# Kernel tuning notes

Hardware: AMD Instinct MI355X
Metric: run time of the kernel (lower is better)

Reference implementation:

```python
import jax, jax.numpy as jnp
import numpy as np

NUM_HEADS = 16


def setup_inputs() -> dict:
    key = jax.random.key(0)
    ks = jax.random.split(key, 7)
    B, L, H = 4, 1370, 1024
    s = 0.02
    return {
        "hidden_states": jax.random.normal(ks[0], (B, L, H), jnp.float32),
        "Wq": jax.random.normal(ks[1], (H, H), jnp.float32) * s,
        "bq": jax.random.normal(ks[2], (H,), jnp.float32) * s,
        "Wk": jax.random.normal(ks[3], (H, H), jnp.float32) * s,
        "bk": jax.random.normal(ks[4], (H,), jnp.float32) * s,
        "Wv": jax.random.normal(ks[5], (H, H), jnp.float32) * s,
        "bv": jax.random.normal(ks[6], (H,), jnp.float32) * s,
    }


def reference(hidden_states, Wq, bq, Wk, bk, Wv, bv):
    B, L, hidden = hidden_states.shape
    n_heads = NUM_HEADS
    d = hidden // n_heads  # head_dim = 64

    def split_heads(x):  # [B,L,hidden] -> [B,H,L,d]
        return x.reshape(B, L, n_heads, d).transpose(0, 2, 1, 3)

    # torch Linear: y = x @ W^T + b
    q = split_heads(hidden_states @ Wq.T + bq)
    k = split_heads(hidden_states @ Wk.T + bk)
    v = split_heads(hidden_states @ Wv.T + bv)

    scale = 1.0 / jnp.sqrt(jnp.asarray(d, hidden_states.dtype))
    # attn_bias is all-zeros (no causal mask, no head_mask) -> omitted
    scores = jnp.einsum("bhld,bhsd->bhls", q, k) * scale  # [B,H,L,S]
    attn = jax.nn.softmax(scores, axis=-1)
    # dropout_p = 0.0 (eval mode), callback is None
    ctx = jnp.einsum("bhls,bhsd->bhld", attn, v)  # [B,H,L,d]
    ctx = ctx.transpose(0, 2, 1, 3).reshape(B, L, hidden)
    return ctx
```

## Files before the change

### kernel.cpp

```cpp
#include <hip/hip_runtime.h>

#define B_    4
#define L_    1370
#define NH_   16
#define D_    64
#define HID_  1024
#define M_    (B_ * L_)
#define LPAD  1408

#define XB_OFF  0u
#define WB_OFF  5611520u
#define QW_OFF  8757248u
#define KW_OFF  14524416u
#define VT_OFF  20291584u

typedef __attribute__((ext_vector_type(8))) short bf16x8;
typedef __attribute__((ext_vector_type(4))) short bf16x4;
typedef __attribute__((ext_vector_type(4))) float f32x4;
typedef __attribute__((ext_vector_type(2))) unsigned int u32x2;

#define LOG2E   1.44269504089f
#define QSCALE  0.18033688011f
#define SOFT_M2 14.4269504089f

__device__ __forceinline__ unsigned short f2bf(float f) {
  unsigned int u = __builtin_bit_cast(unsigned int, f);
  u += 0x7FFFu + ((u >> 16) & 1u);
  return (unsigned short)(u >> 16);
}

__device__ __forceinline__ float fexp2(float x) {
#if __has_builtin(__builtin_amdgcn_exp2f)
  return __builtin_amdgcn_exp2f(x);
#else
  return exp2f(x);
#endif
}

__device__ __forceinline__ unsigned int pkbf(float a, float b) {
#if __has_builtin(__builtin_amdgcn_cvt_pk_bf16_f32)
  auto r = __builtin_amdgcn_cvt_pk_bf16_f32(a, b);
  return __builtin_bit_cast(unsigned int, r);
#else
  return (unsigned int)f2bf(a) | ((unsigned int)f2bf(b) << 16);
#endif
}

#define GLOAD16(gp, lp)                                                    \
  __builtin_amdgcn_global_load_lds(                                        \
      (const __attribute__((address_space(1))) unsigned int*)(gp),         \
      (__attribute__((address_space(3))) unsigned int*)(lp), 16, 0, 0)

#define XN4 ((M_ * HID_) / 4)
#define WN4 ((HID_ * HID_) / 4)
#define TOT4 (XN4 + 3 * WN4)

__global__ void cvt_all(const float* __restrict__ hs,
                        const float* __restrict__ Wq,
                        const float* __restrict__ Wk,
                        const float* __restrict__ Wv,
                        unsigned short* __restrict__ ws) {
  int i4 = blockIdx.x * 256 + threadIdx.x;
  if (i4 >= TOT4) return;
  const float* src;
  unsigned short* dst;
  if (i4 < XN4) {
    src = hs + (size_t)i4 * 4;
    dst = ws + XB_OFF + (size_t)i4 * 4;
  } else {
    int j = i4 - XN4;
    int w = j >> 18;
    int jj = j & (WN4 - 1);
    src = (w == 0 ? Wq : w == 1 ? Wk : Wv) + (size_t)jj * 4;
    dst = ws + WB_OFF + (size_t)w * (HID_ * HID_) + (size_t)jj * 4;
  }
  float4 v = *(const float4*)src;
  bf16x4 o;
  o[0] = (short)f2bf(v.x); o[1] = (short)f2bf(v.y);
  o[2] = (short)f2bf(v.z); o[3] = (short)f2bf(v.w);
  *(bf16x4*)dst = o;
}

__global__ __launch_bounds__(256)
void qkv_gemm(const unsigned short* __restrict__ XB,
              const unsigned short* __restrict__ WB,
              const float* __restrict__ bq,
              const float* __restrict__ bk,
              const float* __restrict__ bv,
              unsigned short* __restrict__ ws) {
  __shared__ unsigned short smem[32768];

  const int x = blockIdx.x;
  const int b = (x >= 33) ? 3 : (x >= 22) ? 2 : (x >= 11) ? 1 : 0;
  const int j = x - 11 * b;
  const int z = blockIdx.z;
  const int n0 = blockIdx.y * 128;

  const unsigned short* W = WB + (size_t)z * (HID_ * HID_);
  const float* bias = (z == 0) ? bq : (z == 1) ? bk : bv;
  const float scale = (z == 0) ? QSCALE : 1.0f;

  const int tid = threadIdx.x;
  const int lane = tid & 63;
  const int wv = tid >> 6;
  const int l15 = lane & 15, quad = lane >> 4;
  const int wr = wv >> 1, wc = wv & 1;

  const int srow = (lane >> 3);
  const int gsw = (lane & 7) ^ srow;
  int offA[4], offB[4];
#pragma unroll
  for (int i = 0; i < 4; ++i) {
    int row = wv * 32 + 8 * i + srow;
    int m = b * L_ + min(j * 128 + row, L_ - 1);
    offA[i] = m * HID_ + gsw * 8;
    offB[i] = (n0 + row) * HID_ + gsw * 8;
  }

  f32x4 acc[4][4];
#pragma unroll
  for (int i = 0; i < 4; i++)
#pragma unroll
    for (int jj = 0; jj < 4; jj++) acc[i][jj] = (f32x4){0.f, 0.f, 0.f, 0.f};

#pragma unroll
  for (int i = 0; i < 4; ++i) {
    GLOAD16(XB + offA[i], &smem[(wv * 32 + 8 * i) * 64]);
    GLOAD16(W + offB[i], &smem[8192 + (wv * 32 + 8 * i) * 64]);
  }

  for (int kt = 0; kt < HID_ / 64; ++kt) {
    __syncthreads();
    unsigned short* cur = smem + (kt & 1) * 16384;
    if (kt + 1 < HID_ / 64) {
      unsigned short* nxt = smem + ((kt + 1) & 1) * 16384;
      const int ko = (kt + 1) * 64;
#pragma unroll
      for (int i = 0; i < 4; ++i) {
        GLOAD16(XB + offA[i] + ko, &nxt[(wv * 32 + 8 * i) * 64]);
        GLOAD16(W + offB[i] + ko, &nxt[8192 + (wv * 32 + 8 * i) * 64]);
      }
    }
    const unsigned short* lA = cur;
    const unsigned short* lB = cur + 8192;
#pragma unroll
    for (int kk = 0; kk < 2; ++kk) {
      bf16x8 af[4], bfr[4];
#pragma unroll
      for (int mi = 0; mi < 4; mi++) {
        int row = wr * 64 + mi * 16 + l15;
        af[mi] = *(const bf16x8*)&lA[row * 64 + (((kk * 4 + quad) ^ (l15 & 7)) * 8)];
      }
#pragma unroll
      for (int ni = 0; ni < 4; ni++) {
        int row = wc * 64 + ni * 16 + l15;
        bfr[ni] = *(const bf16x8*)&lB[row * 64 + (((kk * 4 + quad) ^ (l15 & 7)) * 8)];
      }
#pragma unroll
      for (int mi = 0; mi < 4; mi++)
#pragma unroll
        for (int ni = 0; ni < 4; ni++)
          acc[mi][ni] = __builtin_amdgcn_mfma_f32_16x16x32_bf16(af[mi], bfr[ni], acc[mi][ni], 0, 0, 0);
    }
  }

  __syncthreads();
  unsigned short* lC = smem + wv * 4096;
  const int h = blockIdx.y * 2 + wc;
  const int bh = b * 16 + h;
  const int lbase = j * 128 + wr * 64;

  if (z < 2) {
#pragma unroll
    for (int ni = 0; ni < 4; ni++) {
      int nl = ni * 16 + l15;
      float bn = bias[n0 + wc * 64 + nl];
      int gsn = nl >> 3, en = nl & 7;
#pragma unroll
      for (int mi = 0; mi < 4; mi++)
#pragma unroll
        for (int r = 0; r < 4; r++) {
          int ml = mi * 16 + quad * 4 + r;
          lC[ml * 64 + ((gsn ^ (ml & 7)) * 8) + en] = f2bf((acc[mi][ni][r] + bn) * scale);
        }
    }
    unsigned short* dst = ws + (z == 0 ? QW_OFF : KW_OFF) + (size_t)bh * (LPAD * 64);
#pragma unroll
    for (int i = 0; i < 8; ++i) {
      int ml = i * 8 + (lane >> 3);
      int g = lane & 7;
      bf16x8 v = *(const bf16x8*)&lC[ml * 64 + ((g ^ (ml & 7)) * 8)];
      int l = lbase + ml;
      *(bf16x8*)(dst + (size_t)l * 64 + g * 8) = v;
    }
  } else {
#pragma unroll
    for (int ni = 0; ni < 4; ni++) {
      int nl = ni * 16 + l15;
      float bn = bias[n0 + wc * 64 + nl];
#pragma unroll
      for (int mi = 0; mi < 4; mi++) {
        bf16x4 pk;
#pragma unroll
        for (int r = 0; r < 4; r++) pk[r] = (short)f2bf(acc[mi][ni][r] + bn);
        int gm = mi * 2 + (quad >> 1), h2 = quad & 1;
        *(bf16x4*)&lC[nl * 64 + ((gm ^ (nl & 7)) * 8) + h2 * 4] = pk;
      }
    }
    unsigned short* vt = ws + VT_OFF + (size_t)bh * (64 * LPAD);
#pragma unroll
    for (int i = 0; i < 8; ++i) {
      int nl = i * 8 + (lane >> 3);
      int g = lane & 7;
      bf16x8 v = *(const bf16x8*)&lC[nl * 64 + ((g ^ (nl & 7)) * 8)];
      int l = lbase + g * 8;
      *(bf16x8*)(vt + (size_t)nl * LPAD + l) = v;
    }
  }
}

__global__ __launch_bounds__(256)
void attn(const unsigned short* __restrict__ ws, float* __restrict__ out) {
  __shared__ unsigned short lKV[2 * 8192];
  __shared__ unsigned short lP[4 * 32 * 64];

  const int tid = threadIdx.x;
  const int qt = blockIdx.x >> 3;
  const int bh = blockIdx.y * 8 + (blockIdx.x & 7);
  const int b = bh >> 4, h = bh & 15;
  const int lane = tid & 63, wv = tid >> 6;
  const int l15 = lane & 15, quad = lane >> 4;

  const unsigned short* Qp = ws + QW_OFF + (size_t)bh * (LPAD * 64);
  const unsigned short* Kp = ws + KW_OFF + (size_t)bh * (LPAD * 64);
  const unsigned short* Vt = ws + VT_OFF + (size_t)bh * (64 * LPAD);

  const int srow = lane >> 3;
  const int gsw = (lane & 7) ^ srow;
  const bool isK = (wv < 2);
  const int half = wv & 1;
  const unsigned short* gbase = isK ? Kp : Vt;
  const int lofs = (isK ? 0 : 4096) + half * 32 * 64;
  int goff[4];
#pragma unroll
  for (int t = 0; t < 4; ++t) {
    int row = half * 32 + 8 * t + srow;
    goff[t] = isK ? (row * 64 + gsw * 8)
                  : (row * LPAD + gsw * 8);
  }
  const int gstep = isK ? (64 * 64) : 64;

  bf16x8 qf[2][2];
#pragma unroll
  for (int q2 = 0; q2 < 2; ++q2) {
    int qrow = qt * 128 + wv * 32 + q2 * 16 + l15;
    qf[q2][0] = *(const bf16x8*)(Qp + (size_t)qrow * 64 + quad * 8);
    qf[q2][1] = *(const bf16x8*)(Qp + (size_t)qrow * 64 + 32 + quad * 8);
  }

  bf16x8 ones;
#pragma unroll
  for (int jj = 0; jj < 8; jj++) ones[jj] = (short)0x3F80;

  const f32x4 minit = {-SOFT_M2, -SOFT_M2, -SOFT_M2, -SOFT_M2};

  f32x4 o[2][4], osum[2];
#pragma unroll
  for (int q2 = 0; q2 < 2; q2++) {
    osum[q2] = (f32x4){0.f, 0.f, 0.f, 0.f};
#pragma unroll
    for (int d = 0; d < 4; d++) o[q2][d] = (f32x4){0.f, 0.f, 0.f, 0.f};
  }

  unsigned short* lPw = lP + wv * 2048;

  const int NT = (L_ + 63) / 64;

#pragma unroll
  for (int t = 0; t < 4; ++t)
    GLOAD16(gbase + goff[t], lKV + lofs + t * 512);

  for (int kt = 0; kt < NT; ++kt) {
    const int s0 = kt * 64;
    __syncthreads();
    const unsigned short* lK = lKV + (kt & 1) * 8192;
    const unsigned short* lV = lK + 4096;
    if (kt + 1 < NT) {
      unsigned short* nxt = lKV + ((kt + 1) & 1) * 8192 + lofs;
      const int go = (kt + 1) * gstep;
#pragma unroll
      for (int t = 0; t < 4; ++t)
        GLOAD16(gbase + goff[t] + go, nxt + t * 512);
    }

#pragma unroll
    for (int cb = 0; cb < 4; cb++) {
      int krow = cb * 16 + l15;
      bf16x8 kf0 = *(const bf16x8*)&lK[krow * 64 + ((quad ^ (l15 & 7)) * 8)];
      bf16x8 kf1 = *(const bf16x8*)&lK[krow * 64 + (((4 + quad) ^ (l15 & 7)) * 8)];
#pragma unroll
      for (int q2 = 0; q2 < 2; q2++) {
        f32x4 a = minit;
        a = __builtin_amdgcn_mfma_f32_16x16x32_bf16(kf0, qf[q2][0], a, 0, 0, 0);
        a = __builtin_amdgcn_mfma_f32_16x16x32_bf16(kf1, qf[q2][1], a, 0, 0, 0);
        if (s0 + 64 > L_) {
#pragma unroll
          for (int r = 0; r < 4; r++)
            if (s0 + cb * 16 + quad * 4 + r >= L_) a[r] = -1e30f;
        }
        u32x2 pk;
        pk[0] = pkbf(fexp2(a[0]), fexp2(a[1]));
        pk[1] = pkbf(fexp2(a[2]), fexp2(a[3]));
        int prow = q2 * 16 + l15;
        int gw = cb * 2 + (quad >> 1), h2 = quad & 1;
        *(u32x2*)&lPw[prow * 64 + ((gw ^ (l15 & 7)) * 8) + h2 * 4] = pk;
      }
    }

#pragma unroll
    for (int kk = 0; kk < 2; kk++) {
      bf16x8 pa[2];
#pragma unroll
      for (int q2 = 0; q2 < 2; q2++) {
        pa[q2] = *(const bf16x8*)&lPw[(q2 * 16 + l15) * 64 + (((kk * 4 + quad) ^ (l15 & 7)) * 8)];
        osum[q2] = __builtin_amdgcn_mfma_f32_16x16x32_bf16(pa[q2], ones, osum[q2], 0, 0, 0);
      }
#pragma unroll
      for (int d = 0; d < 4; d++) {
        int vrow = d * 16 + l15;
        bf16x8 vb = *(const bf16x8*)&lV[vrow * 64 + (((kk * 4 + quad) ^ (l15 & 7)) * 8)];
#pragma unroll
        for (int q2 = 0; q2 < 2; q2++)
          o[q2][d] = __builtin_amdgcn_mfma_f32_16x16x32_bf16(pa[q2], vb, o[q2][d], 0, 0, 0);
      }
    }
  }

#pragma unroll
  for (int q2 = 0; q2 < 2; q2++) {
    float inv[4];
#pragma unroll
    for (int r = 0; r < 4; r++) inv[r] = 1.0f / osum[q2][r];
#pragma unroll
    for (int d = 0; d < 4; d++)
#pragma unroll
      for (int r = 0; r < 4; r++) {
        int l = qt * 128 + wv * 32 + q2 * 16 + quad * 4 + r;
        if (l < L_) {
          int dd = d * 16 + l15;
          out[((size_t)(b * L_ + l)) * HID_ + h * 64 + dd] = o[q2][d][r] * inv[r];
        }
      }
  }
}

extern "C" void kernel_launch(void* const* d_in, const int* in_sizes, int n_in,
                              void* d_out, int out_size, void* d_ws, size_t ws_size,
                              hipStream_t stream) {
  const float* hs = (const float*)d_in[0];
  const float* Wq = (const float*)d_in[1];
  const float* bq = (const float*)d_in[2];
  const float* Wk = (const float*)d_in[3];
  const float* bk = (const float*)d_in[4];
  const float* Wv = (const float*)d_in[5];
  const float* bv = (const float*)d_in[6];
  float* out = (float*)d_out;
  unsigned short* ws = (unsigned short*)d_ws;

  cvt_all<<<dim3((TOT4 + 255) / 256), 256, 0, stream>>>(hs, Wq, Wk, Wv, ws);

  qkv_gemm<<<dim3(44, 8, 3), 256, 0, stream>>>(ws + XB_OFF, ws + WB_OFF,
                                               bq, bk, bv, ws);

  attn<<<dim3(88, 8), 256, 0, stream>>>(ws, out);
}
```

Measured before the change: 194.0 us.

## Halve GEMM K-tile to cut LDS and pad Q buffer for more attention tiles

```diff
diff --git a/kernel.cpp b/kernel.cpp
--- a/kernel.cpp
+++ b/kernel.cpp
@@ -7,12 +7,13 @@
 #define HID_  1024
 #define M_    (B_ * L_)
 #define LPAD  1408
+#define QPAD  1536
 
 #define XB_OFF  0u
 #define WB_OFF  5611520u
 #define QW_OFF  8757248u
-#define KW_OFF  14524416u
-#define VT_OFF  20291584u
+#define KW_OFF  15048704u
+#define VT_OFF  20815872u
 
 typedef __attribute__((ext_vector_type(8))) short bf16x8;
 typedef __attribute__((ext_vector_type(4))) short bf16x4;
@@ -88,7 +89,7 @@
               const float* __restrict__ bk,
               const float* __restrict__ bv,
               unsigned short* __restrict__ ws) {
-  __shared__ unsigned short smem[32768];
+  __shared__ unsigned short smem[16384];
 
   const int x = blockIdx.x;
   const int b = (x >= 33) ? 3 : (x >= 22) ? 2 : (x >= 11) ? 1 : 0;
@@ -106,15 +107,15 @@
   const int l15 = lane & 15, quad = lane >> 4;
   const int wr = wv >> 1, wc = wv & 1;
 
-  const int srow = (lane >> 3);
-  const int gsw = (lane & 7) ^ srow;
-  int offA[4], offB[4];
-#pragma unroll
-  for (int i = 0; i < 4; ++i) {
-    int row = wv * 32 + 8 * i + srow;
+  const int srow = lane >> 2;
+  const int gsw = (lane & 3) ^ (srow & 3);
+  int offA[2], offB[2];
+#pragma unroll
+  for (int t = 0; t < 2; ++t) {
+    int row = wv * 32 + t * 16 + srow;
     int m = b * L_ + min(j * 128 + row, L_ - 1);
-    offA[i] = m * HID_ + gsw * 8;
-    offB[i] = (n0 + row) * HID_ + gsw * 8;
+    offA[t] = m * HID_ + gsw * 8;
+    offB[t] = (n0 + row) * HID_ + gsw * 8;
   }
 
   f32x4 acc[4][4];
@@ -124,44 +125,41 @@
     for (int jj = 0; jj < 4; jj++) acc[i][jj] = (f32x4){0.f, 0.f, 0.f, 0.f};
 
 #pragma unroll
-  for (int i = 0; i < 4; ++i) {
-    GLOAD16(XB + offA[i], &smem[(wv * 32 + 8 * i) * 64]);
-    GLOAD16(W + offB[i], &smem[8192 + (wv * 32 + 8 * i) * 64]);
-  }
-
-  for (int kt = 0; kt < HID_ / 64; ++kt) {
+  for (int t = 0; t < 2; ++t) {
+    GLOAD16(XB + offA[t], &smem[(wv * 32 + t * 16) * 32]);
+    GLOAD16(W + offB[t], &smem[4096 + (wv * 32 + t * 16) * 32]);
+  }
+
+  for (int kt = 0; kt < HID_ / 32; ++kt) {
     __syncthreads();
-    unsigned short* cur = smem + (kt & 1) * 16384;
-    if (kt + 1 < HID_ / 64) {
-      unsigned short* nxt = smem + ((kt + 1) & 1) * 16384;
-      const int ko = (kt + 1) * 64;
-#pragma unroll
-      for (int i = 0; i < 4; ++i) {
-        GLOAD16(XB + offA[i] + ko, &nxt[(wv * 32 + 8 * i) * 64]);
-        GLOAD16(W + offB[i] + ko, &nxt[8192 + (wv * 32 + 8 * i) * 64]);
+    const unsigned short* cur = smem + (kt & 1) * 8192;
+    if (kt + 1 < HID_ / 32) {
+      unsigned short* nxt = smem + ((kt + 1) & 1) * 8192;
+      const int ko = (kt + 1) * 32;
+#pragma unroll
+      for (int t = 0; t < 2; ++t) {
+        GLOAD16(XB + offA[t] + ko, &nxt[(wv * 32 + t * 16) * 32]);
+        GLOAD16(W + offB[t] + ko, &nxt[4096 + (wv * 32 + t * 16) * 32]);
       }
     }
     const unsigned short* lA = cur;
-    const unsigned short* lB = cur + 8192;
-#pragma unroll
-    for (int kk = 0; kk < 2; ++kk) {
-      bf16x8 af[4], bfr[4];
-#pragma unroll
-      for (int mi = 0; mi < 4; mi++) {
-        int row = wr * 64 + mi * 16 + l15;
-        af[mi] = *(const bf16x8*)&lA[row * 64 + (((kk * 4 + quad) ^ (l15 & 7)) * 8)];
-      }
-#pragma unroll
-      for (int ni = 0; ni < 4; ni++) {
-        int row = wc * 64 + ni * 16 + l15;
-        bfr[ni] = *(const bf16x8*)&lB[row * 64 + (((kk * 4 + quad) ^ (l15 & 7)) * 8)];
-      }
-#pragma unroll
-      for (int mi = 0; mi < 4; mi++)
-#pragma unroll
-        for (int ni = 0; ni < 4; ni++)
-          acc[mi][ni] = __builtin_amdgcn_mfma_f32_16x16x32_bf16(af[mi], bfr[ni], acc[mi][ni], 0, 0, 0);
-    }
+    const unsigned short* lB = cur + 4096;
+    bf16x8 af[4], bfr[4];
+#pragma unroll
+    for (int mi = 0; mi < 4; mi++) {
+      int row = wr * 64 + mi * 16 + l15;
+      af[mi] = *(const bf16x8*)&lA[row * 32 + ((quad ^ (l15 & 3)) * 8)];
+    }
+#pragma unroll
+    for (int ni = 0; ni < 4; ni++) {
+      int row = wc * 64 + ni * 16 + l15;
+      bfr[ni] = *(const bf16x8*)&lB[row * 32 + ((quad ^ (l15 & 3)) * 8)];
+    }
+#pragma unroll
+    for (int mi = 0; mi < 4; mi++)
+#pragma unroll
+      for (int ni = 0; ni < 4; ni++)
+        acc[mi][ni] = __builtin_amdgcn_mfma_f32_16x16x32_bf16(af[mi], bfr[ni], acc[mi][ni], 0, 0, 0);
   }
 
   __syncthreads();
@@ -184,7 +182,8 @@
           lC[ml * 64 + ((gsn ^ (ml & 7)) * 8) + en] = f2bf((acc[mi][ni][r] + bn) * scale);
         }
     }
-    unsigned short* dst = ws + (z == 0 ? QW_OFF : KW_OFF) + (size_t)bh * (LPAD * 64);
+    unsigned short* dst = ws + (z == 0 ? QW_OFF : KW_OFF) +
+                          (size_t)bh * ((z == 0 ? QPAD : LPAD) * 64);
 #pragma unroll
     for (int i = 0; i < 8; ++i) {
       int ml = i * 8 + (lane >> 3);
@@ -231,7 +230,7 @@
   const int lane = tid & 63, wv = tid >> 6;
   const int l15 = lane & 15, quad = lane >> 4;
 
-  const unsigned short* Qp = ws + QW_OFF + (size_t)bh * (LPAD * 64);
+  const unsigned short* Qp = ws + QW_OFF + (size_t)bh * (QPAD * 64);
   const unsigned short* Kp = ws + KW_OFF + (size_t)bh * (LPAD * 64);
   const unsigned short* Vt = ws + VT_OFF + (size_t)bh * (64 * LPAD);
 
@@ -372,5 +371,5 @@
   qkv_gemm<<<dim3(44, 8, 3), 256, 0, stream>>>(ws + XB_OFF, ws + WB_OFF,
                                                bq, bk, bv, ws);
 
-  attn<<<dim3(88, 8), 256, 0, stream>>>(ws, out);
-}
+  attn<<<dim3(96, 8), 256, 0, stream>>>(ws, out);
+}
```

Result: slower. 203.1 us (+4.7%).
